# Kernel tuning notes

Hardware: AMD Instinct MI355X
Metric: run time of the kernel (lower is better)

## Reference

```python
import jax, jax.numpy as jnp
import numpy as np

N = 50000
E = 800000
DIM = 256
HEADS = 4
HDIM = DIM // HEADS  # 64
NEG_SLOPE = 0.2
LN_EPS = 1e-5


def _layernorm(x, g, b):
    mu = jnp.mean(x, axis=-1, keepdims=True)
    var = jnp.var(x, axis=-1, keepdims=True)
    return (x - mu) * jax.lax.rsqrt(var + LN_EPS) * g + b


def setup_inputs() -> dict:
    key = jax.random.key(0)
    ks = jax.random.split(key, 10)
    x = jax.random.normal(ks[0], (N, DIM), dtype=jnp.float32)
    edge_index = jax.random.randint(ks[1], (2, E), 0, N, dtype=jnp.int64)
    s = 0.05
    W = jax.random.normal(ks[2], (DIM, DIM), dtype=jnp.float32) * s       # GAT linear (heads*out = dim)
    a_src = jax.random.normal(ks[3], (HEADS, HDIM), dtype=jnp.float32) * s
    a_dst = jax.random.normal(ks[4], (HEADS, HDIM), dtype=jnp.float32) * s
    gat_b = jnp.zeros((DIM,), dtype=jnp.float32)
    ln_g = jnp.ones((DIM,), dtype=jnp.float32)
    ln_b = jnp.zeros((DIM,), dtype=jnp.float32)
    W1 = jax.random.normal(ks[5], (DIM, 4 * DIM), dtype=jnp.float32) * s
    b1 = jnp.zeros((4 * DIM,), dtype=jnp.float32)
    W2 = jax.random.normal(ks[6], (4 * DIM, DIM), dtype=jnp.float32) * s
    b2 = jnp.zeros((DIM,), dtype=jnp.float32)
    return {"x": x, "edge_index": edge_index, "W": W, "a_src": a_src,
            "a_dst": a_dst, "gat_b": gat_b, "ln_g": ln_g, "ln_b": ln_b,
            "W1": W1, "b1": b1, "W2": W2, "b2": b2}


def _gat(x, edge_index, W, a_src, a_dst, gat_b):
    # project and split heads: [N, H, C]
    h = (x @ W).reshape(N, HEADS, HDIM)
    alpha_src = jnp.einsum('nhc,hc->nh', h, a_src)  # [N, H]
    alpha_dst = jnp.einsum('nhc,hc->nh', h, a_dst)  # [N, H]
    src = edge_index[0]
    dst = edge_index[1]
    e = jax.nn.leaky_relu(alpha_src[src] + alpha_dst[dst], NEG_SLOPE)  # [E, H]
    # segment softmax over edges sharing a destination node
    m = jax.ops.segment_max(e, dst, num_segments=N)                   # [N, H]
    ex = jnp.exp(e - m[dst])
    denom = jax.ops.segment_sum(ex, dst, num_segments=N)              # [N, H]
    alpha = ex / (denom[dst] + 1e-16)                                 # [E, H]
    msg = h[src] * alpha[:, :, None]                                  # [E, H, C]
    out = jax.ops.segment_sum(msg.reshape(E, DIM), dst, num_segments=N)
    return out + gat_b


def reference(x, edge_index, W, a_src, a_dst, gat_b, ln_g, ln_b, W1, b1, W2, b2):
    residual = x
    g = _gat(x, edge_index, W, a_src, a_dst, gat_b)
    x = _layernorm(x + g, ln_g, ln_b)
    ffn = jax.nn.gelu(x @ W1 + b1, approximate=False) @ W2 + b2
    x = _layernorm(x + ffn, ln_g, ln_b)  # same norm params reused, as in source
    return x + residual
```

## Files before the change

### kernel.cpp

```cpp
#include <hip/hip_runtime.h>
#include <hip/hip_bf16.h>
#include <math.h>

typedef __bf16 bf16;
typedef bf16 bf16x8 __attribute__((ext_vector_type(8)));
typedef float floatx4 __attribute__((ext_vector_type(4)));

#define NN 50000
#define EE 800000
#define DIMC 256
#define FFC 1024

typedef __attribute__((address_space(3))) unsigned int lds_u32;
typedef __attribute__((address_space(1))) unsigned int gbl_u32;

static __device__ __forceinline__ void glds16(const bf16* g, bf16* l) {
    __builtin_amdgcn_global_load_lds((const gbl_u32*)g, (lds_u32*)l, 16, 0, 0);
}

static __device__ __forceinline__ unsigned short f2b(float f) {
    bf16 b = (bf16)f;
    return __builtin_bit_cast(unsigned short, b);
}
static __device__ __forceinline__ float b2f_lo(unsigned u) { return __uint_as_float(u << 16); }
static __device__ __forceinline__ float b2f_hi(unsigned u) { return __uint_as_float(u & 0xffff0000u); }

static __device__ __forceinline__ float gelu_f(float v) {
    float z = -1.5957691216f * v - 0.0713548163f * v * v * v;
    return v / (1.f + __expf(z));
}

__global__ __launch_bounds__(256)
void k_cast_count(const float* __restrict__ in, bf16* __restrict__ out, long n4,
                  const int* __restrict__ dst, unsigned* __restrict__ deg) {
    long i = (long)blockIdx.x * 256 + threadIdx.x;
    if (i < EE) atomicAdd(&deg[dst[(int)i]], 1u);
    if (i >= n4) return;
    float4 v = ((const float4*)in)[i];
    uint2 p;
    p.x = (unsigned)f2b(v.x) | ((unsigned)f2b(v.y) << 16);
    p.y = (unsigned)f2b(v.z) | ((unsigned)f2b(v.w) << 16);
    ((uint2*)out)[i] = p;
}

__global__ __launch_bounds__(256)
void k_tcast_all(const float* __restrict__ W, bf16* __restrict__ WT,
                 const float* __restrict__ W1, bf16* __restrict__ W1T,
                 const float* __restrict__ W2, bf16* __restrict__ W2T) {
    __shared__ float t[32][33];
    int b = blockIdx.x;
    const float* in; bf16* out; int K, Nc, bx, by;
    if (b < 64)        { in = W;  out = WT;  K = 256;  Nc = 256;  bx = b & 7;  by = b >> 3; }
    else if (b < 320)  { b -= 64;  in = W1; out = W1T; K = 256;  Nc = 1024; bx = b & 31; by = b >> 5; }
    else               { b -= 320; in = W2; out = W2T; K = 1024; Nc = 256;  bx = b & 7;  by = b >> 3; }
    int n0 = bx * 32, k0 = by * 32;
    int tx = threadIdx.x & 31, ty = threadIdx.x >> 5;
#pragma unroll
    for (int i = 0; i < 4; ++i)
        t[ty + i * 8][tx] = in[(long)(k0 + ty + i * 8) * Nc + n0 + tx];
    __syncthreads();
#pragma unroll
    for (int i = 0; i < 4; ++i)
        out[(long)(n0 + ty + i * 8) * K + k0 + tx] = (bf16)t[tx][ty + i * 8];
}

template <int EPI>
__global__ __launch_bounds__(256)
void k_gemmA(const bf16* __restrict__ A, const bf16* __restrict__ BT,
             bf16* __restrict__ C, const float* __restrict__ bias,
             const float* __restrict__ avs, const float* __restrict__ avd,
             float* __restrict__ asrcO, float* __restrict__ adstO,
             int M, int K, int Nc) {
    __shared__ __attribute__((aligned(16))) bf16 smem[17408];
    bf16* As = smem;
    bf16* Bs = smem + 8192;
    const int tid = threadIdx.x;
    const int w = tid >> 6, lane = tid & 63;
    const int gm = blockIdx.x * 128, gn = blockIdx.y * 128;
    const int wm = (w >> 1) * 64, wn = (w & 1) * 64;
    const int lr = lane & 15, lkc = lane >> 4;

    long aoff[4], boff[4];
#pragma unroll
    for (int j = 0; j < 4; ++j) {
        int s = w * 4 + j;
        int r = s * 8 + (lane >> 3);
        int kc = ((lane & 7) ^ (r & 7)) * 8;
        aoff[j] = (long)min(gm + r, M - 1) * K + kc;
        boff[j] = (long)(gn + r) * K + kc;
    }

    floatx4 acc[4][4];
#pragma unroll
    for (int a = 0; a < 4; ++a)
#pragma unroll
        for (int b = 0; b < 4; ++b) acc[a][b] = floatx4{0.f, 0.f, 0.f, 0.f};

    for (int k0 = 0; k0 < K; k0 += 64) {
        if (k0) __syncthreads();
#pragma unroll
        for (int j = 0; j < 4; ++j) {
            int s = w * 4 + j;
            glds16(A + aoff[j] + k0, As + s * 512);
            glds16(BT + boff[j] + k0, Bs + s * 512);
        }
        __syncthreads();
#pragma unroll
        for (int kk = 0; kk < 2; ++kk) {
            bf16x8 af[4], bv[4];
#pragma unroll
            for (int mi = 0; mi < 4; ++mi) {
                int r = wm + mi * 16 + lr;
                int ch = (kk * 4 + lkc) ^ (r & 7);
                af[mi] = *(const bf16x8*)(As + r * 64 + ch * 8);
            }
#pragma unroll
            for (int ni = 0; ni < 4; ++ni) {
                int r = wn + ni * 16 + lr;
                int ch = (kk * 4 + lkc) ^ (r & 7);
                bv[ni] = *(const bf16x8*)(Bs + r * 64 + ch * 8);
            }
#pragma unroll
            for (int mi = 0; mi < 4; ++mi)
#pragma unroll
                for (int ni = 0; ni < 4; ++ni)
                    acc[mi][ni] = __builtin_amdgcn_mfma_f32_16x16x32_bf16(af[mi], bv[ni], acc[mi][ni], 0, 0, 0);
        }
    }

    __syncthreads();
    bf16* cs = smem;
#pragma unroll
    for (int ni = 0; ni < 4; ++ni) {
        const int cl = wn + ni * 16 + lr;
        const float bvs = (EPI == 1) ? bias[gn + cl] : 0.f;
#pragma unroll
        for (int mi = 0; mi < 4; ++mi)
#pragma unroll
            for (int i = 0; i < 4; ++i) {
                int rl = wm + mi * 16 + lkc * 4 + i;
                float v = acc[mi][ni][i] + bvs;
                if (EPI == 1) v = gelu_f(v);
                cs[rl * 136 + cl] = (bf16)v;
            }
    }
    __syncthreads();

    const int c8 = (lane & 15) * 8;
    float as8[8], ad8[8];
    int hd = 0;
    if (EPI == 0) {
        hd = (gn >> 6) + ((lane & 15) >> 3);
        const int cb = hd * 64 + (c8 & 63);
#pragma unroll
        for (int i = 0; i < 8; ++i) { as8[i] = avs[cb + i]; ad8[i] = avd[cb + i]; }
    }

#pragma unroll
    for (int t = 0; t < 8; ++t) {
        int rl = w * 32 + t * 4 + (lane >> 4);
        int grow = gm + rl;
        uint4 val = *(const uint4*)(cs + rl * 136 + c8);
        if (grow < M) *(uint4*)(C + (long)grow * Nc + gn + c8) = val;
        if (EPI == 0) {
            float h0 = b2f_lo(val.x), h1 = b2f_hi(val.x), h2 = b2f_lo(val.y), h3 = b2f_hi(val.y);
            float h4 = b2f_lo(val.z), h5 = b2f_hi(val.z), h6 = b2f_lo(val.w), h7 = b2f_hi(val.w);
            float ds = h0 * as8[0] + h1 * as8[1] + h2 * as8[2] + h3 * as8[3]
                     + h4 * as8[4] + h5 * as8[5] + h6 * as8[6] + h7 * as8[7];
            float dd = h0 * ad8[0] + h1 * ad8[1] + h2 * ad8[2] + h3 * ad8[3]
                     + h4 * ad8[4] + h5 * ad8[5] + h6 * ad8[6] + h7 * ad8[7];
#pragma unroll
            for (int off = 1; off < 8; off <<= 1) { ds += __shfl_xor(ds, off); dd += __shfl_xor(dd, off); }
            if ((lane & 7) == 0 && grow < M) {
                asrcO[grow * 4 + hd] = ds;
                adstO[grow * 4 + hd] = dd;
            }
        }
    }
}

#define STAGE_W(cc, pp) do {                                                    \
    bf16* w1d = smem + 4096 + (pp) * 8192;                                      \
    bf16* w2d = smem + 20480 + (pp) * 8192;                                     \
    _Pragma("unroll")                                                           \
    for (int j = 0; j < 2; ++j) {                                               \
        int sg = w * 2 + j;                                                     \
        int r = sg * 2 + (lane >> 5);                                           \
        int col = ((lane & 31) ^ (r & 7)) * 8;                                  \
        glds16(W1T + (long)((cc) * 32 + r) * DIMC + col, w1d + sg * 512);       \
    }                                                                           \
    _Pragma("unroll")                                                           \
    for (int j = 0; j < 2; ++j) {                                               \
        int sg = w * 2 + j;                                                     \
        int r = sg * 16 + (lane >> 2);                                          \
        int col = (cc) * 32 + (((lane & 3) ^ ((r >> 1) & 3)) * 8);              \
        glds16(W2T + (long)r * FFC + col, w2d + sg * 512);                      \
    }                                                                           \
} while (0)

__global__ __launch_bounds__(512)
void k_ffn(const bf16* __restrict__ x1b, const bf16* __restrict__ W1T,
           const bf16* __restrict__ W2T, const float* __restrict__ b1,
           const float* __restrict__ b2, const float* __restrict__ x,
           const float* __restrict__ lng, const float* __restrict__ lnb,
           float* __restrict__ out, int M) {
    __shared__ __attribute__((aligned(16))) bf16 smem[36864];
    float* actf = (float*)smem;
    const int tid = threadIdx.x;
    const int w = tid >> 6, lane = tid & 63;
    const int lr = lane & 15, lkc = lane >> 4;
    const int mg = w >> 1, nh = w & 1;
    const int gm = blockIdx.x * 64;

    bf16x8 xf[8];
    {
        long rb = (long)min(gm + mg * 16 + lr, M - 1) * DIMC;
#pragma unroll
        for (int kf = 0; kf < 8; ++kf)
            xf[kf] = *(const bf16x8*)(x1b + rb + kf * 32 + lkc * 8);
    }

    floatx4 accB[8];
#pragma unroll
    for (int i = 0; i < 8; ++i) accB[i] = floatx4{0.f, 0.f, 0.f, 0.f};

    const int rbA = nh * 16 + lr;
    const int rAct = mg * 16 + lr;
    const int kAct = nh * 16 + lr;

    STAGE_W(0, 0);

    for (int c = 0; c < 32; ++c) {
        const int p = c & 1;
        __syncthreads();
        if (c < 31) STAGE_W(c + 1, p ^ 1);
        bf16* w1s = smem + 4096 + p * 8192;
        bf16* w2s = smem + 20480 + p * 8192;

        floatx4 a0 = floatx4{0.f, 0.f, 0.f, 0.f}, a1 = a0;
#pragma unroll
        for (int kf = 0; kf < 8; kf += 2) {
            int g0 = (kf * 4 + lkc) ^ (rbA & 7);
            int g1 = ((kf + 1) * 4 + lkc) ^ (rbA & 7);
            bf16x8 bva = *(const bf16x8*)(w1s + rbA * 256 + g0 * 8);
            bf16x8 bvb = *(const bf16x8*)(w1s + rbA * 256 + g1 * 8);
            a0 = __builtin_amdgcn_mfma_f32_16x16x32_bf16(xf[kf], bva, a0, 0, 0, 0);
            a1 = __builtin_amdgcn_mfma_f32_16x16x32_bf16(xf[kf + 1], bvb, a1, 0, 0, 0);
        }
        float b1v = b1[c * 32 + kAct];
#pragma unroll
        for (int i = 0; i < 4; ++i) {
            int r = mg * 16 + lkc * 4 + i;
            float v = gelu_f(a0[i] + a1[i] + b1v);
            actf[r * 32 + (((kAct >> 2) ^ (r & 7)) << 2) + (kAct & 3)] = v;
        }
        asm volatile("s_waitcnt lgkmcnt(0)" ::: "memory");
        __builtin_amdgcn_s_barrier();
        asm volatile("" ::: "memory");

        {
            int g0 = (lkc * 2) ^ (rAct & 7);
            int g1 = (lkc * 2 + 1) ^ (rAct & 7);
            float4 lo = *(const float4*)(actf + rAct * 32 + g0 * 4);
            float4 hi = *(const float4*)(actf + rAct * 32 + g1 * 4);
            bf16x8 af;
            af[0] = (bf16)lo.x; af[1] = (bf16)lo.y; af[2] = (bf16)lo.z; af[3] = (bf16)lo.w;
            af[4] = (bf16)hi.x; af[5] = (bf16)hi.y; af[6] = (bf16)hi.z; af[7] = (bf16)hi.w;
#pragma unroll
            for (int ni = 0; ni < 8; ++ni) {
                int rb = nh * 128 + ni * 16 + lr;
                int gb = lkc ^ ((rb >> 1) & 3);
                bf16x8 bv = *(const bf16x8*)(w2s + rb * 32 + gb * 8);
                accB[ni] = __builtin_amdgcn_mfma_f32_16x16x32_bf16(af, bv, accB[ni], 0, 0, 0);
            }
        }
    }

    __syncthreads();
    bf16* cs = smem;
#pragma unroll
    for (int ni = 0; ni < 8; ++ni) {
        int col = nh * 128 + ni * 16 + lr;
        float b2v = b2[col];
#pragma unroll
        for (int i = 0; i < 4; ++i) {
            int rl = mg * 16 + lkc * 4 + i;
            cs[rl * 264 + col] = (bf16)(accB[ni][i] + b2v);
        }
    }
    __syncthreads();
    float4 g4 = *(const float4*)(lng + lane * 4);
    float4 lb4 = *(const float4*)(lnb + lane * 4);
#pragma unroll 1
    for (int t = 0; t < 8; ++t) {
        int r = w * 8 + t;
        int grow = gm + r;
        long base = (long)min(grow, M - 1) * DIMC + lane * 4;
        uint2 cu = *(const uint2*)(cs + r * 264 + lane * 4);
        uint2 xu = *(const uint2*)(x1b + base);
        float v0 = b2f_lo(cu.x) + b2f_lo(xu.x);
        float v1 = b2f_hi(cu.x) + b2f_hi(xu.x);
        float v2 = b2f_lo(cu.y) + b2f_lo(xu.y);
        float v3 = b2f_hi(cu.y) + b2f_hi(xu.y);
        float s1 = v0 + v1 + v2 + v3;
        float s2 = v0 * v0 + v1 * v1 + v2 * v2 + v3 * v3;
#pragma unroll
        for (int off = 1; off < 64; off <<= 1) { s1 += __shfl_xor(s1, off); s2 += __shfl_xor(s2, off); }
        float mu = s1 * (1.f / DIMC);
        float rs = rsqrtf(s2 * (1.f / DIMC) - mu * mu + 1e-5f);
        float4 xr = *(const float4*)(x + base);
        float4 o;
        o.x = (v0 - mu) * rs * g4.x + lb4.x + xr.x;
        o.y = (v1 - mu) * rs * g4.y + lb4.y + xr.y;
        o.z = (v2 - mu) * rs * g4.z + lb4.z + xr.z;
        o.w = (v3 - mu) * rs * g4.w + lb4.w + xr.w;
        if (grow < M) *(float4*)(out + (long)grow * DIMC + lane * 4) = o;
    }
}

__global__ __launch_bounds__(1024)
void k_scan1(const unsigned* __restrict__ deg, unsigned* __restrict__ rowoff,
             unsigned* __restrict__ cursor, unsigned* __restrict__ bsum) {
    __shared__ unsigned wsum[16], wscan[16];
    int tid = threadIdx.x, lane = tid & 63, wid = tid >> 6;
    int i = blockIdx.x * 1024 + tid;
    unsigned v = (i < NN) ? deg[i] : 0u;
    unsigned s = v;
    for (int off = 1; off < 64; off <<= 1) {
        unsigned t = __shfl_up(s, off);
        if (lane >= off) s += t;
    }
    if (lane == 63) wsum[wid] = s;
    __syncthreads();
    if (wid == 0) {
        unsigned t = (lane < 16) ? wsum[lane] : 0u;
        unsigned ts = t;
        for (int off = 1; off < 16; off <<= 1) {
            unsigned u2 = __shfl_up(ts, off);
            if (lane >= off) ts += u2;
        }
        if (lane < 16) wscan[lane] = ts;
    }
    __syncthreads();
    unsigned basew = (wid > 0) ? wscan[wid - 1] : 0u;
    unsigned excl = basew + (s - v);
    if (i < NN) { rowoff[i] = excl; cursor[i] = excl; }
    if (tid == 0) bsum[blockIdx.x] = wscan[15];
}

__global__ __launch_bounds__(64)
void k_scan2(unsigned* __restrict__ bsum, unsigned* __restrict__ rowoff) {
    int lane = threadIdx.x;
    unsigned v = (lane < 49) ? bsum[lane] : 0u;
    unsigned s = v;
    for (int off = 1; off < 64; off <<= 1) {
        unsigned t = __shfl_up(s, off);
        if (lane >= off) s += t;
    }
    if (lane < 49) bsum[lane] = s - v;
    if (lane == 48) rowoff[NN] = s;
}

__global__ __launch_bounds__(256)
void k_scan3(const unsigned* __restrict__ bsum, unsigned* __restrict__ rowoff,
             unsigned* __restrict__ cursor) {
    int i = blockIdx.x * 256 + threadIdx.x;
    if (i < NN) {
        unsigned o = bsum[i >> 10];
        rowoff[i] += o;
        cursor[i] += o;
    }
}

__global__ __launch_bounds__(256)
void k_fill(const int* __restrict__ src, const int* __restrict__ dst,
            const float* __restrict__ asrc, unsigned* __restrict__ cursor,
            unsigned* __restrict__ elist, float4* __restrict__ evals) {
    int e = blockIdx.x * 256 + threadIdx.x;
    if (e < EE) {
        int s = src[e];
        unsigned p = atomicAdd(&cursor[dst[e]], 1u);
        elist[p] = (unsigned)s;
        evals[p] = *(const float4*)(asrc + (long)s * 4);
    }
}

__global__ __launch_bounds__(256)
void k_agg_ln1(const unsigned* __restrict__ rowoff, const unsigned* __restrict__ elist,
               const float* __restrict__ evals, const float* __restrict__ adst,
               const bf16* __restrict__ hb, const float* __restrict__ x,
               const float* __restrict__ gatb, const float* __restrict__ lng,
               const float* __restrict__ lnb, bf16* __restrict__ x1b) {
    int node = (blockIdx.x * 256 + threadIdx.x) >> 6;
    int lane = threadIdx.x & 63;
    if (node >= NN) return;
    int beg = (int)rowoff[node], end = (int)rowoff[node + 1];
    int head = lane >> 4;
    float ad = adst[node * 4 + head];
    const int c = lane * 4;
    const bf16* hc = hb + c;
    const int bl = lane & 48;

    float dsum = 0.f;
    float a0 = 0.f, a1 = 0.f, a2 = 0.f, a3 = 0.f;

    for (int c0 = beg; c0 < end; c0 += 16) {
        int take = end - c0; if (take > 16) take = 16;
        int jj = c0 + (lane & 15);
        float ex = 0.f; int s = 0;
        if (jj < end) {
            s = (int)elist[jj];
            float e = evals[(long)jj * 4 + head] + ad;
            e = (e > 0.f) ? e : 0.2f * e;
            ex = __expf(e);
        }
        dsum += ex;
        if (take == 16) {
#pragma unroll
            for (int j = 0; j < 16; ++j) {
                float al = __shfl(ex, bl + j);
                int sj = __shfl(s, bl + j);
                uint2 u = *(const uint2*)(hc + (long)sj * DIMC);
                a0 += al * b2f_lo(u.x);
                a1 += al * b2f_hi(u.x);
                a2 += al * b2f_lo(u.y);
                a3 += al * b2f_hi(u.y);
            }
        } else {
            for (int j = 0; j < take; ++j) {
                float al = __shfl(ex, bl + j);
                int sj = __shfl(s, bl + j);
                uint2 u = *(const uint2*)(hc + (long)sj * DIMC);
                a0 += al * b2f_lo(u.x);
                a1 += al * b2f_hi(u.x);
                a2 += al * b2f_lo(u.y);
                a3 += al * b2f_hi(u.y);
            }
        }
    }
    dsum += __shfl_xor(dsum, 1);
    dsum += __shfl_xor(dsum, 2);
    dsum += __shfl_xor(dsum, 4);
    dsum += __shfl_xor(dsum, 8);
    float invd = 1.f / (dsum + 1e-16f);
    a0 *= invd; a1 *= invd; a2 *= invd; a3 *= invd;

    long base = (long)node * DIMC + c;
    float4 xr = *(const float4*)(x + base);
    float4 gb = *(const float4*)(gatb + c);
    float v0 = xr.x + a0 + gb.x;
    float v1 = xr.y + a1 + gb.y;
    float v2 = xr.z + a2 + gb.z;
    float v3 = xr.w + a3 + gb.w;
    float s1 = v0 + v1 + v2 + v3;
    float s2 = v0 * v0 + v1 * v1 + v2 * v2 + v3 * v3;
    for (int off = 1; off < 64; off <<= 1) { s1 += __shfl_xor(s1, off); s2 += __shfl_xor(s2, off); }
    float mu = s1 * (1.f / DIMC);
    float rs = rsqrtf(s2 * (1.f / DIMC) - mu * mu + 1e-5f);
    float4 g4 = *(const float4*)(lng + c);
    float4 b4 = *(const float4*)(lnb + c);
    float y0 = (v0 - mu) * rs * g4.x + b4.x;
    float y1 = (v1 - mu) * rs * g4.y + b4.y;
    float y2 = (v2 - mu) * rs * g4.z + b4.z;
    float y3 = (v3 - mu) * rs * g4.w + b4.w;
    uint2 p;
    p.x = (unsigned)f2b(y0) | ((unsigned)f2b(y1) << 16);
    p.y = (unsigned)f2b(y2) | ((unsigned)f2b(y3) << 16);
    *(uint2*)(x1b + base) = p;
}

extern "C" void kernel_launch(void* const* d_in, const int* in_sizes, int n_in,
                              void* d_out, int out_size, void* d_ws, size_t ws_size,
                              hipStream_t stream) {
    const float* x    = (const float*)d_in[0];
    const int*   ei   = (const int*)d_in[1];
    const float* W    = (const float*)d_in[2];
    const float* a_s  = (const float*)d_in[3];
    const float* a_d  = (const float*)d_in[4];
    const float* gatb = (const float*)d_in[5];
    const float* lng  = (const float*)d_in[6];
    const float* lnb  = (const float*)d_in[7];
    const float* W1   = (const float*)d_in[8];
    const float* b1   = (const float*)d_in[9];
    const float* W2   = (const float*)d_in[10];
    const float* b2   = (const float*)d_in[11];
    float* out = (float*)d_out;
    char* ws = (char*)d_ws;

    bf16*     xb     = (bf16*)(ws + 0L);
    bf16*     hb     = (bf16*)(ws + 25600000L);
    bf16*     x1b    = (bf16*)(ws + 51200000L);
    unsigned* bsum   = (unsigned*)(ws + 76800000L);
    float4*   evals  = (float4*)(ws + 77000032L);
    float*    asrc   = (float*)(ws + 179200000L);
    float*    adst   = (float*)(ws + 180000000L);
    unsigned* deg    = (unsigned*)(ws + 180800000L);
    unsigned* cursor = (unsigned*)(ws + 181000192L);
    unsigned* rowoff = (unsigned*)(ws + 181200384L);
    unsigned* elist  = (unsigned*)(ws + 181400832L);
    bf16*     WT     = (bf16*)(ws + 184600832L);
    bf16*     W1T    = (bf16*)(ws + 184731904L);
    bf16*     W2T    = (bf16*)(ws + 185256192L);

    const int* esrc = ei;
    const int* edst = ei + EE;

    hipMemsetAsync(deg, 0, NN * sizeof(unsigned), stream);
    k_cast_count<<<12500, 256, 0, stream>>>(x, xb, (long)NN * DIMC / 4, edst, deg);
    k_tcast_all<<<576, 256, 0, stream>>>(W, WT, W1, W1T, W2, W2T);

    dim3 g1(391, 2);
    k_gemmA<0><<<g1, 256, 0, stream>>>(xb, WT, hb, nullptr, a_s, a_d, asrc, adst, NN, DIMC, DIMC);

    k_scan1<<<49, 1024, 0, stream>>>(deg, rowoff, cursor, bsum);
    k_scan2<<<1, 64, 0, stream>>>(bsum, rowoff);
    k_scan3<<<196, 256, 0, stream>>>(bsum, rowoff, cursor);
    k_fill<<<3125, 256, 0, stream>>>(esrc, edst, asrc, cursor, elist, evals);

    k_agg_ln1<<<12500, 256, 0, stream>>>(rowoff, elist, (const float*)evals, adst, hb, x, gatb, lng, lnb, x1b);

    k_ffn<<<782, 512, 0, stream>>>(x1b, W1T, W2T, b1, b2, x, lng, lnb, out, NN);
}
```

Baseline: 441.7 us.

## Widen FFN hidden chunk to 64 and drop double-buffered weight staging

The fused FFN kernel now processes 64 hidden units per iteration instead of 32, which halves the loop trip count and the number of barriers. Each wave computes two 16-wide hidden tiles, and the second GEMM does two K=32 MFMAs per output tile. The double-buffered prefetch of W1/W2 is replaced by a single buffer loaded synchronously at the top of each iteration, so weight loads no longer overlap with compute. This trades latency hiding for fewer synchronisation points and larger per-iteration work.

```diff
diff --git a/kernel.cpp b/kernel.cpp
--- a/kernel.cpp
+++ b/kernel.cpp
@@ -179,22 +179,20 @@
     }
 }
 
-#define STAGE_W(cc, pp) do {                                                    \
-    bf16* w1d = smem + 4096 + (pp) * 8192;                                      \
-    bf16* w2d = smem + 20480 + (pp) * 8192;                                     \
+#define STAGE_W64(cc) do {                                                      \
     _Pragma("unroll")                                                           \
-    for (int j = 0; j < 2; ++j) {                                               \
-        int sg = w * 2 + j;                                                     \
+    for (int j = 0; j < 4; ++j) {                                               \
+        int sg = w * 4 + j;                                                     \
         int r = sg * 2 + (lane >> 5);                                           \
-        int col = ((lane & 31) ^ (r & 7)) * 8;                                  \
-        glds16(W1T + (long)((cc) * 32 + r) * DIMC + col, w1d + sg * 512);       \
+        int g = (lane & 31) ^ (r & 7);                                          \
+        glds16(W1T + (long)((cc) * 64 + r) * DIMC + g * 8, w1s + sg * 512);     \
     }                                                                           \
     _Pragma("unroll")                                                           \
-    for (int j = 0; j < 2; ++j) {                                               \
-        int sg = w * 2 + j;                                                     \
-        int r = sg * 16 + (lane >> 2);                                          \
-        int col = (cc) * 32 + (((lane & 3) ^ ((r >> 1) & 3)) * 8);              \
-        glds16(W2T + (long)r * FFC + col, w2d + sg * 512);                      \
+    for (int j = 0; j < 4; ++j) {                                               \
+        int sg = w * 4 + j;                                                     \
+        int r = sg * 8 + (lane >> 3);                                           \
+        int g = (lane & 7) ^ ((r >> 1) & 7);                                    \
+        glds16(W2T + (long)r * FFC + (cc) * 64 + g * 8, w2s + sg * 512);        \
     }                                                                           \
 } while (0)
 
@@ -204,8 +202,10 @@
            const float* __restrict__ b2, const float* __restrict__ x,
            const float* __restrict__ lng, const float* __restrict__ lnb,
            float* __restrict__ out, int M) {
-    __shared__ __attribute__((aligned(16))) bf16 smem[36864];
+    __shared__ __attribute__((aligned(16))) bf16 smem[40960];
     float* actf = (float*)smem;
+    bf16* w1s = smem + 8192;
+    bf16* w2s = smem + 24576;
     const int tid = threadIdx.x;
     const int w = tid >> 6, lane = tid & 63;
     const int lr = lane & 15, lkc = lane >> 4;
@@ -224,55 +224,59 @@
 #pragma unroll
     for (int i = 0; i < 8; ++i) accB[i] = floatx4{0.f, 0.f, 0.f, 0.f};
 
-    const int rbA = nh * 16 + lr;
+    const int rb0 = nh * 32 + lr;
+    const int rb1 = nh * 32 + 16 + lr;
     const int rAct = mg * 16 + lr;
-    const int kAct = nh * 16 + lr;
-
-    STAGE_W(0, 0);
-
-    for (int c = 0; c < 32; ++c) {
-        const int p = c & 1;
+
+    for (int c = 0; c < 16; ++c) {
+        if (c) __syncthreads();
+        STAGE_W64(c);
         __syncthreads();
-        if (c < 31) STAGE_W(c + 1, p ^ 1);
-        bf16* w1s = smem + 4096 + p * 8192;
-        bf16* w2s = smem + 20480 + p * 8192;
 
         floatx4 a0 = floatx4{0.f, 0.f, 0.f, 0.f}, a1 = a0;
 #pragma unroll
-        for (int kf = 0; kf < 8; kf += 2) {
-            int g0 = (kf * 4 + lkc) ^ (rbA & 7);
-            int g1 = ((kf + 1) * 4 + lkc) ^ (rbA & 7);
-            bf16x8 bva = *(const bf16x8*)(w1s + rbA * 256 + g0 * 8);
-            bf16x8 bvb = *(const bf16x8*)(w1s + rbA * 256 + g1 * 8);
-            a0 = __builtin_amdgcn_mfma_f32_16x16x32_bf16(xf[kf], bva, a0, 0, 0, 0);
-            a1 = __builtin_amdgcn_mfma_f32_16x16x32_bf16(xf[kf + 1], bvb, a1, 0, 0, 0);
-        }
-        float b1v = b1[c * 32 + kAct];
+        for (int kf = 0; kf < 8; ++kf) {
+            int g = kf * 4 + lkc;
+            bf16x8 bv0 = *(const bf16x8*)(w1s + rb0 * 256 + ((g ^ (rb0 & 7)) * 8));
+            bf16x8 bv1 = *(const bf16x8*)(w1s + rb1 * 256 + ((g ^ (rb1 & 7)) * 8));
+            a0 = __builtin_amdgcn_mfma_f32_16x16x32_bf16(xf[kf], bv0, a0, 0, 0, 0);
+            a1 = __builtin_amdgcn_mfma_f32_16x16x32_bf16(xf[kf], bv1, a1, 0, 0, 0);
+        }
+        float b1v0 = b1[c * 64 + nh * 32 + lr];
+        float b1v1 = b1[c * 64 + nh * 32 + 16 + lr];
+        float* ah = actf + nh * 2048;
 #pragma unroll
         for (int i = 0; i < 4; ++i) {
             int r = mg * 16 + lkc * 4 + i;
-            float v = gelu_f(a0[i] + a1[i] + b1v);
-            actf[r * 32 + (((kAct >> 2) ^ (r & 7)) << 2) + (kAct & 3)] = v;
-        }
-        asm volatile("s_waitcnt lgkmcnt(0)" ::: "memory");
-        __builtin_amdgcn_s_barrier();
-        asm volatile("" ::: "memory");
-
+            int e0 = lr, e1 = 16 + lr;
+            ah[r * 32 + (((e0 >> 2) ^ (r & 7)) << 2) + (e0 & 3)] = gelu_f(a0[i] + b1v0);
+            ah[r * 32 + (((e1 >> 2) ^ (r & 7)) << 2) + (e1 & 3)] = gelu_f(a1[i] + b1v1);
+        }
+        __syncthreads();
+
+        bf16x8 af0, af1;
         {
             int g0 = (lkc * 2) ^ (rAct & 7);
             int g1 = (lkc * 2 + 1) ^ (rAct & 7);
-            float4 lo = *(const float4*)(actf + rAct * 32 + g0 * 4);
-            float4 hi = *(const float4*)(actf + rAct * 32 + g1 * 4);
-            bf16x8 af;
-            af[0] = (bf16)lo.x; af[1] = (bf16)lo.y; af[2] = (bf16)lo.z; af[3] = (bf16)lo.w;
-            af[4] = (bf16)hi.x; af[5] = (bf16)hi.y; af[6] = (bf16)hi.z; af[7] = (bf16)hi.w;
-#pragma unroll
-            for (int ni = 0; ni < 8; ++ni) {
-                int rb = nh * 128 + ni * 16 + lr;
-                int gb = lkc ^ ((rb >> 1) & 3);
-                bf16x8 bv = *(const bf16x8*)(w2s + rb * 32 + gb * 8);
-                accB[ni] = __builtin_amdgcn_mfma_f32_16x16x32_bf16(af, bv, accB[ni], 0, 0, 0);
-            }
+            const float* h0p = actf;
+            const float* h1p = actf + 2048;
+            float4 lo = *(const float4*)(h0p + rAct * 32 + g0 * 4);
+            float4 hi = *(const float4*)(h0p + rAct * 32 + g1 * 4);
+            af0[0] = (bf16)lo.x; af0[1] = (bf16)lo.y; af0[2] = (bf16)lo.z; af0[3] = (bf16)lo.w;
+            af0[4] = (bf16)hi.x; af0[5] = (bf16)hi.y; af0[6] = (bf16)hi.z; af0[7] = (bf16)hi.w;
+            lo = *(const float4*)(h1p + rAct * 32 + g0 * 4);
+            hi = *(const float4*)(h1p + rAct * 32 + g1 * 4);
+            af1[0] = (bf16)lo.x; af1[1] = (bf16)lo.y; af1[2] = (bf16)lo.z; af1[3] = (bf16)lo.w;
+            af1[4] = (bf16)hi.x; af1[5] = (bf16)hi.y; af1[6] = (bf16)hi.z; af1[7] = (bf16)hi.w;
+        }
+#pragma unroll
+        for (int ni = 0; ni < 8; ++ni) {
+            int rb = nh * 128 + ni * 16 + lr;
+            int sw = (rb >> 1) & 7;
+            bf16x8 bv0 = *(const bf16x8*)(w2s + rb * 64 + ((lkc ^ sw) * 8));
+            bf16x8 bv1 = *(const bf16x8*)(w2s + rb * 64 + (((4 + lkc) ^ sw) * 8));
+            accB[ni] = __builtin_amdgcn_mfma_f32_16x16x32_bf16(af0, bv0, accB[ni], 0, 0, 0);
+            accB[ni] = __builtin_amdgcn_mfma_f32_16x16x32_bf16(af1, bv1, accB[ni], 0, 0, 0);
         }
     }
 
```

New measurement: 513.7 us. 16.3% more time.
